# Kernel optimization log

Hardware: AMD Instinct MI355X
Metric: run time of the kernel (lower is better)

The kernel has to match this reference:

```python
import jax, jax.numpy as jnp
import numpy as np

THRESHOLD = 0.75
MIN_TOKENS = 128
POOL_OUT = 128
EPS = 1e-5


def setup_inputs() -> dict:
    key = jax.random.key(0)
    k1, k2 = jax.random.split(key)
    B, T, N, D = 64, 6, 128, 768
    A = 51
    return {
        "features_event": jax.random.normal(k1, (B, T, N, D), dtype=jnp.float32),
        "ln_gamma": jnp.ones((D,), jnp.float32),
        "ln_beta": jnp.zeros((D,), jnp.float32),
        "w_attr": jax.random.normal(k2, (A, D), dtype=jnp.float32) * 0.02,
        "b_attr": jnp.zeros((A,), jnp.float32),
        "bn_gamma": jnp.ones((A,), jnp.float32),
        "bn_beta": jnp.zeros((A,), jnp.float32),
    }


def _filter_and_pool(x):
    # x: [B, TN, D] -> [B, POOL_OUT, D], faithful to
    # filter_similar_tokens_vectorized + pad_sequence + AdaptiveAvgPool1d(128).
    B, TN, D = x.shape
    x_norm = x / jnp.linalg.norm(x, axis=-1, keepdims=True)
    sim = jnp.einsum('bid,bjd->bij', x_norm, x_norm)          # [B, TN, TN]
    high = (sim > THRESHOLD) & ~jnp.eye(TN, dtype=bool)[None]
    keep = ~jnp.any(high, axis=2)                             # [B, TN]
    counts = jnp.sum(keep, axis=1)
    # per-sample fallback: if fewer than MIN_TOKENS survive, keep top-k by L2 norm
    scores = jnp.linalg.norm(x, axis=-1)                      # [B, TN]
    _, topk_idx = jax.lax.top_k(scores, MIN_TOKENS)
    topk_mask = jnp.zeros((B, TN), bool).at[jnp.arange(B)[:, None], topk_idx].set(True)
    keep = jnp.where((counts < MIN_TOKENS)[:, None], topk_mask, keep)
    counts = jnp.sum(keep, axis=1)                            # per-sample kept length
    L = jnp.max(counts)                                       # pad_sequence length (traced scalar)
    # stable compaction: kept tokens first, original order preserved; zeros after
    order = jnp.argsort(~keep, axis=1, stable=True)           # [B, TN]
    xs = jnp.take_along_axis(x, order[:, :, None], axis=1)
    pos = jnp.arange(TN)
    xs = jnp.where(pos[None, :, None] < counts[:, None, None], xs, 0.0)
    # AdaptiveAvgPool1d(POOL_OUT) over the first L columns (zeros beyond each
    # sample's count are included, exactly as torch pools the padded tensor).
    # Identity when L == POOL_OUT (each bin holds exactly one element).
    i = jnp.arange(POOL_OUT)
    start = (i * L) // POOL_OUT
    end = ((i + 1) * L + POOL_OUT - 1) // POOL_OUT            # ceil div
    W = ((pos[None, :] >= start[:, None]) & (pos[None, :] < end[:, None])).astype(x.dtype)
    W = W / (end - start)[:, None].astype(x.dtype)            # [POOL_OUT, TN]
    return jnp.einsum('oj,bjd->bod', W, xs)                   # [B, POOL_OUT, D]


def reference(features_event, ln_gamma, ln_beta, w_attr, b_attr, bn_gamma, bn_beta):
    B, T, N, D = features_event.shape
    x = features_event.reshape(B, T * N, D)
    x = _filter_and_pool(x)                                   # [B, 128, D]
    # LayerNorm(dim)
    mu = jnp.mean(x, axis=-1, keepdims=True)
    var = jnp.var(x, axis=-1, keepdims=True)
    x = (x - mu) * jax.lax.rsqrt(var + EPS) * ln_gamma + ln_beta
    # per-attribute Linear(dim, 1) heads fused into one batched matmul
    A = w_attr.shape[0]
    logits = jnp.einsum('bad,ad->ba', x[:, :A, :], w_attr) + b_attr
    # BatchNorm1d(attr_num), training-mode batch statistics
    bm = jnp.mean(logits, axis=0)
    bv = jnp.var(logits, axis=0)
    return (logits - bm) * jax.lax.rsqrt(bv + EPS) * bn_gamma + bn_beta
```

## Files before the change

kernel.cpp:

```cpp
#include <hip/hip_runtime.h>
#include <hip/hip_bf16.h>

#define TN 768
#define DIM 768
#define NB 64
#define NA 51
#define POOL 128
#define THRESH 0.75f
#define LNEPS 1e-5f

typedef float f32x4 __attribute__((ext_vector_type(4)));
typedef long l64x2 __attribute__((ext_vector_type(2)));

typedef const __attribute__((address_space(1))) unsigned int* gas_p;
typedef __attribute__((address_space(3))) unsigned int* las_p;

__device__ __forceinline__ void gload16(const void* g, void* l) {
    __builtin_amdgcn_global_load_lds((gas_p)g, (las_p)l, 16, 0, 0);
}

__constant__ int PAIR_I[21] = {0,1,1,2,2,2,3,3,3,3,4,4,4,4,4,5,5,5,5,5,5};
__constant__ int PAIR_J[21] = {0,0,1,0,1,2,0,1,2,3,0,1,2,3,4,0,1,2,3,4,5};

__global__ __launch_bounds__(256) void k_norms(const float* __restrict__ x,
                                               unsigned int* __restrict__ xn,
                                               float* __restrict__ norms,
                                               int* __restrict__ bad,
                                               int* __restrict__ Lval) {
    if (blockIdx.x < 192) bad[blockIdx.x * 256 + threadIdx.x] = 0;
    if (blockIdx.x == 0 && threadIdx.x == 0) *Lval = 0;

    const int tok  = blockIdx.x * 4 + (threadIdx.x >> 6);
    const int lane = threadIdx.x & 63;
    const float4* p = (const float4*)(x + (size_t)tok * DIM);
    float4 v[3];
    float s = 0.f;
#pragma unroll
    for (int q = 0; q < 3; ++q) {
        v[q] = p[q * 64 + lane];
        s += v[q].x * v[q].x + v[q].y * v[q].y + v[q].z * v[q].z + v[q].w * v[q].w;
    }
#pragma unroll
    for (int m = 1; m < 64; m <<= 1) s += __shfl_xor(s, m);
    const float nrm = sqrtf(s);
    const float sc = 1.0f / nrm;
    unsigned int* xrow = xn + (size_t)tok * 192;
#pragma unroll
    for (int q = 0; q < 3; ++q) {
        int w0 = __builtin_amdgcn_cvt_pk_fp8_f32(v[q].x * sc, v[q].y * sc, 0, false);
        w0     = __builtin_amdgcn_cvt_pk_fp8_f32(v[q].z * sc, v[q].w * sc, w0, true);
        const int k  = q * 256 + lane * 4;
        const int kb = k & 127;
        const int c  = kb >> 5, sl = (kb >> 3) & 3, r = kb & 7;
        const int pos = (k & ~127) + 16 * (4 * (c >> 1) + sl) + 8 * (c & 1) + r;
        xrow[pos >> 2] = (unsigned)w0;
    }
    if (lane == 0) norms[tok] = nrm;
}

__global__ __launch_bounds__(256) void k_gram(const unsigned char* __restrict__ xn,
                                              int* __restrict__ bad) {
    const int f = blockIdx.x;
    const int lid = (f & 7) * 168 + (f >> 3);
    const int b = lid / 21, p = lid - b * 21;
    const int it = PAIR_I[p], jt = PAIR_J[p];
    const bool diag = (it == jt);

    const int tid = threadIdx.x;
    const int lane = tid & 63, w = tid >> 6;
    const int lr = lane & 15, lt = lane >> 4;
    const int wr = w >> 1, wc = w & 1;

    __shared__ alignas(16) unsigned char lA[2][128 * 128];
    __shared__ alignas(16) unsigned char lB[2][128 * 128];

    const unsigned char* xb = xn + (size_t)b * TN * DIM;
    const int srow = lane >> 3;
    const int sgoff = 16 * ((lane & 7) ^ (srow & 7));
    const size_t baseA = (size_t)(jt * 128 + srow) * DIM + sgoff;
    const size_t baseB = (size_t)(it * 128 + srow) * DIM + sgoff;

    f32x4 acc[4][4];
#pragma unroll
    for (int m = 0; m < 4; ++m)
#pragma unroll
        for (int n = 0; n < 4; ++n) acc[m][n] = {0.f, 0.f, 0.f, 0.f};

    auto stage = [&](int bb, int kk) {
#pragma unroll
        for (int i = 0; i < 4; ++i) {
            const int seg = w * 4 + i;
            gload16(xb + baseA + (size_t)seg * 8 * DIM + kk * 128,
                    (char*)lA[bb] + seg * 1024);
        }
        if (!diag) {
#pragma unroll
            for (int i = 0; i < 4; ++i) {
                const int seg = w * 4 + i;
                gload16(xb + baseB + (size_t)seg * 8 * DIM + kk * 128,
                        (char*)lB[bb] + seg * 1024);
            }
        }
    };

    auto compute = [&](int bb) {
        const unsigned char* As = lA[bb];
        const unsigned char* Bs = diag ? lA[bb] : lB[bb];
        const int gx = lr & 7;
#pragma unroll
        for (int q = 0; q < 2; ++q) {
            const int goff = 16 * ((4 * q + lt) ^ gx);
            l64x2 a[4], bv[4];
#pragma unroll
            for (int m = 0; m < 4; ++m)
                a[m] = *(const l64x2*)&As[(wr * 64 + m * 16 + lr) * 128 + goff];
#pragma unroll
            for (int n = 0; n < 4; ++n)
                bv[n] = *(const l64x2*)&Bs[(wc * 64 + n * 16 + lr) * 128 + goff];
#pragma unroll
            for (int m = 0; m < 4; ++m)
#pragma unroll
                for (int n = 0; n < 4; ++n) {
                    acc[m][n] = __builtin_amdgcn_mfma_f32_16x16x32_fp8_fp8(a[m][0], bv[n][0], acc[m][n], 0, 0, 0);
                    acc[m][n] = __builtin_amdgcn_mfma_f32_16x16x32_fp8_fp8(a[m][1], bv[n][1], acc[m][n], 0, 0, 0);
                }
        }
    };

    stage(0, 0);
    asm volatile("s_waitcnt vmcnt(0)" ::: "memory");
    __builtin_amdgcn_s_barrier();
#pragma unroll
    for (int kk = 0; kk < 6; ++kk) {
        const int cur = kk & 1;
        if (kk < 5) stage(cur ^ 1, kk + 1);
        compute(cur);
        if (kk < 5) {
            asm volatile("s_waitcnt vmcnt(0)" ::: "memory");
            __builtin_amdgcn_s_barrier();
        }
    }

#pragma unroll
    for (int m = 0; m < 4; ++m) {
#pragma unroll
        for (int r = 0; r < 4; ++r) {
            const int rowg = jt * 128 + wr * 64 + m * 16 + lt * 4 + r;
            bool any = false;
#pragma unroll
            for (int n = 0; n < 4; ++n) {
                const int colg = it * 128 + wc * 64 + n * 16 + lr;
                any = any || (acc[m][n][r] > THRESH && rowg != colg);
            }
            if (any) bad[b * TN + rowg] = 1;
        }
    }
    if (!diag) {
#pragma unroll
        for (int n = 0; n < 4; ++n) {
            const int colg = it * 128 + wc * 64 + n * 16 + lr;
            bool any = false;
#pragma unroll
            for (int m = 0; m < 4; ++m)
#pragma unroll
                for (int r = 0; r < 4; ++r)
                    any = any || (acc[m][n][r] > THRESH);
            if (any) bad[b * TN + colg] = 1;
        }
    }
}

__global__ __launch_bounds__(256) void k_filter(const int* __restrict__ bad,
                                                const float* __restrict__ norms,
                                                int* __restrict__ inv,
                                                int* __restrict__ counts,
                                                int* __restrict__ Lval) {
    const int b = blockIdx.x, t = threadIdx.x;
    const int w = t >> 6, l = t & 63;
    __shared__ unsigned long long kw[12];
    __shared__ float nsh[TN];

    bool kp[3];
#pragma unroll
    for (int q = 0; q < 3; ++q)
        kp[q] = (bad[b * TN + q * 256 + w * 64 + l] == 0);
#pragma unroll
    for (int q = 0; q < 3; ++q) {
        unsigned long long m = __ballot(kp[q]);
        if (l == 0) kw[4 * q + w] = m;
    }
    __syncthreads();
    int total = 0;
    for (int i = 0; i < 12; ++i) total += __popcll(kw[i]);

    if (total < POOL) {
        for (int j = t; j < TN; j += 256) nsh[j] = norms[b * TN + j];
        __syncthreads();
#pragma unroll
        for (int q = 0; q < 3; ++q) {
            const int j = q * 256 + w * 64 + l;
            const float nj = nsh[j];
            int rank = 0;
            for (int i = 0; i < TN; ++i) {
                float ni = nsh[i];
                rank += (ni > nj) || (ni == nj && i < j);
            }
            kp[q] = (rank < POOL);
        }
        __syncthreads();
#pragma unroll
        for (int q = 0; q < 3; ++q) {
            unsigned long long m = __ballot(kp[q]);
            if (l == 0) kw[4 * q + w] = m;
        }
        __syncthreads();
        total = 0;
        for (int i = 0; i < 12; ++i) total += __popcll(kw[i]);
    }

#pragma unroll
    for (int q = 0; q < 3; ++q) {
        if (kp[q]) {
            const int W = 4 * q + w;
            int pos = __popcll(kw[W] & ((1ull << l) - 1ull));
            for (int i = 0; i < W; ++i) pos += __popcll(kw[i]);
            inv[b * TN + pos] = q * 256 + w * 64 + l;
        }
    }
    if (t == 0) { counts[b] = total; atomicMax(Lval, total); }
}

__device__ inline float block_sum3(float v, volatile float* sred, int t) {
#pragma unroll
    for (int m = 1; m < 64; m <<= 1) v += __shfl_xor(v, m);
    if ((t & 63) == 0) sred[t >> 6] = v;
    __syncthreads();
    float r = sred[0] + sred[1] + sred[2];
    __syncthreads();
    return r;
}

__global__ __launch_bounds__(192) void k_head(const float* __restrict__ x,
                                              const int* __restrict__ inv,
                                              const int* __restrict__ counts,
                                              const int* __restrict__ Lval,
                                              const float* __restrict__ lng,
                                              const float* __restrict__ lnb,
                                              const float* __restrict__ wat,
                                              const float* __restrict__ bat,
                                              float* __restrict__ logits) {
    const int a = blockIdx.x, b = blockIdx.y, t = threadIdx.x;
    __shared__ float sred[3];
    const int L = *Lval, cnt = counts[b];
    const int start = (a * L) >> 7;
    const int end = ((a + 1) * L + 127) >> 7;
    const int wdt = end - start;
    const int pe = min(end, cnt);
    const int nv = pe - start;

    int idx[7];
#pragma unroll
    for (int i = 0; i < 7; ++i)
        idx[i] = (i < nv) ? inv[b * TN + start + i] : 0;

    float4 v[7];
#pragma unroll
    for (int i = 0; i < 7; ++i)
        if (i < nv)
            v[i] = ((const float4*)(x + (size_t)(b * TN + idx[i]) * DIM))[t];

    float4 s4 = {0.f, 0.f, 0.f, 0.f};
#pragma unroll
    for (int i = 0; i < 7; ++i)
        if (i < nv) {
            s4.x += v[i].x; s4.y += v[i].y; s4.z += v[i].z; s4.w += v[i].w;
        }
    const float iw = 1.0f / (float)wdt;
    s4.x *= iw; s4.y *= iw; s4.z *= iw; s4.w *= iw;

    float s1 = block_sum3(s4.x + s4.y + s4.z + s4.w, sred, t);
    float s2 = block_sum3(s4.x * s4.x + s4.y * s4.y + s4.z * s4.z + s4.w * s4.w, sred, t);
    const float mu = s1 * (1.0f / 768.0f);
    const float var = s2 * (1.0f / 768.0f) - mu * mu;
    const float rstd = rsqrtf(var + LNEPS);

    const float4 g  = ((const float4*)lng)[t];
    const float4 be = ((const float4*)lnb)[t];
    const float4 wv = ((const float4*)(wat + (size_t)a * DIM))[t];
    float d = ((s4.x - mu) * rstd * g.x + be.x) * wv.x
            + ((s4.y - mu) * rstd * g.y + be.y) * wv.y
            + ((s4.z - mu) * rstd * g.z + be.z) * wv.z
            + ((s4.w - mu) * rstd * g.w + be.w) * wv.w;
    float dot = block_sum3(d, sred, t);
    if (t == 0) logits[b * NA + a] = dot + bat[a];
}

__global__ __launch_bounds__(64) void k_bn(const float* __restrict__ logits,
                                           const float* __restrict__ bng,
                                           const float* __restrict__ bnb,
                                           float* __restrict__ out) {
    const int a = threadIdx.x;
    if (a >= NA) return;
    float s = 0.f, s2 = 0.f;
    for (int b = 0; b < NB; ++b) {
        float v = logits[b * NA + a];
        s += v; s2 += v * v;
    }
    const float m = s * (1.0f / 64.0f);
    const float var = s2 * (1.0f / 64.0f) - m * m;
    const float rstd = rsqrtf(var + LNEPS);
    const float ga = bng[a], be = bnb[a];
    for (int b = 0; b < NB; ++b)
        out[b * NA + a] = (logits[b * NA + a] - m) * rstd * ga + be;
}

extern "C" void kernel_launch(void* const* d_in, const int* in_sizes, int n_in,
                              void* d_out, int out_size, void* d_ws, size_t ws_size,
                              hipStream_t stream) {
    const float* x     = (const float*)d_in[0];
    const float* ln_g  = (const float*)d_in[1];
    const float* ln_b  = (const float*)d_in[2];
    const float* w_at  = (const float*)d_in[3];
    const float* b_at  = (const float*)d_in[4];
    const float* bn_g  = (const float*)d_in[5];
    const float* bn_b  = (const float*)d_in[6];
    float* out = (float*)d_out;

    char* wsc = (char*)d_ws;
    const size_t XN = 64ull * 768 * 768;
    unsigned char* xn = (unsigned char*)wsc;
    float* norms  = (float*)(wsc + XN);
    int*   bad    = (int*)(wsc + XN + 196608);
    int*   inv    = (int*)(wsc + XN + 393216);
    int*   counts = (int*)(wsc + XN + 589824);
    int*   Lval   = (int*)(wsc + XN + 590080);
    float* logits = (float*)(wsc + XN + 590336);

    k_norms <<<NB * TN / 4, 256, 0, stream>>>(x, (unsigned int*)xn, norms, bad, Lval);
    k_gram  <<<21 * NB, 256, 0, stream>>>(xn, bad);
    k_filter<<<NB, 256, 0, stream>>>(bad, norms, inv, counts, Lval);
    k_head  <<<dim3(NA, NB), 192, 0, stream>>>(x, inv, counts, Lval,
                                               ln_g, ln_b, w_at, b_at, logits);
    k_bn    <<<1, 64, 0, stream>>>(logits, bn_g, bn_b, out);
}
```

Baseline: 76.98 us.

## Make gram kernel persistent over 2-3 tile pairs with cross-tile prefetch

The Gram kernel now launches 512 blocks instead of one block per tile pair, and each block walks 2 or 3 consecutive (batch, tile-pair) items. While it computes the last K-chunk of one tile it prefetches the first chunk of the next, which hides the per-tile prologue load and evens out the tail across CUs. The fp8 normalized rows are now stored in plain order instead of the permuted MFMA-friendly layout. This is still correct because both operands read the same layout and the dot product ignores a consistent K permutation, and it removes index math in k_norms. The trade-offs are fewer blocks in flight and some serialization of the epilogue inside each block.

```diff
diff --git a/kernel.cpp b/kernel.cpp
--- a/kernel.cpp
+++ b/kernel.cpp
@@ -49,22 +49,19 @@
     for (int q = 0; q < 3; ++q) {
         int w0 = __builtin_amdgcn_cvt_pk_fp8_f32(v[q].x * sc, v[q].y * sc, 0, false);
         w0     = __builtin_amdgcn_cvt_pk_fp8_f32(v[q].z * sc, v[q].w * sc, w0, true);
-        const int k  = q * 256 + lane * 4;
-        const int kb = k & 127;
-        const int c  = kb >> 5, sl = (kb >> 3) & 3, r = kb & 7;
-        const int pos = (k & ~127) + 16 * (4 * (c >> 1) + sl) + 8 * (c & 1) + r;
-        xrow[pos >> 2] = (unsigned)w0;
+        xrow[q * 64 + lane] = (unsigned)w0;
     }
     if (lane == 0) norms[tok] = nrm;
 }
+
+struct PS { const unsigned char* pA; const unsigned char* pB; int b, it, jt, diag; };
 
 __global__ __launch_bounds__(256) void k_gram(const unsigned char* __restrict__ xn,
                                               int* __restrict__ bad) {
-    const int f = blockIdx.x;
-    const int lid = (f & 7) * 168 + (f >> 3);
-    const int b = lid / 21, p = lid - b * 21;
-    const int it = PAIR_I[p], jt = PAIR_J[p];
-    const bool diag = (it == jt);
+    const int blk = blockIdx.x;
+    const int chunk = (blk & 7) * 64 + (blk >> 3);
+    const int np     = (chunk < 320) ? 3 : 2;
+    const int pstart = (chunk < 320) ? chunk * 3 : 960 + (chunk - 320) * 2;
 
     const int tid = threadIdx.x;
     const int lane = tid & 63, w = tid >> 6;
@@ -74,38 +71,40 @@
     __shared__ alignas(16) unsigned char lA[2][128 * 128];
     __shared__ alignas(16) unsigned char lB[2][128 * 128];
 
-    const unsigned char* xb = xn + (size_t)b * TN * DIM;
     const int srow = lane >> 3;
     const int sgoff = 16 * ((lane & 7) ^ (srow & 7));
-    const size_t baseA = (size_t)(jt * 128 + srow) * DIM + sgoff;
-    const size_t baseB = (size_t)(it * 128 + srow) * DIM + sgoff;
-
-    f32x4 acc[4][4];
-#pragma unroll
-    for (int m = 0; m < 4; ++m)
-#pragma unroll
-        for (int n = 0; n < 4; ++n) acc[m][n] = {0.f, 0.f, 0.f, 0.f};
-
-    auto stage = [&](int bb, int kk) {
+
+    auto mkstate = [&](int idx, PS& s) {
+        const int lid = pstart + idx;
+        const int b = lid / 21, p = lid - b * 21;
+        s.b = b; s.it = PAIR_I[p]; s.jt = PAIR_J[p]; s.diag = (s.it == s.jt);
+        const unsigned char* xb = xn + (size_t)b * TN * DIM;
+        s.pA = xb + (size_t)(s.jt * 128 + srow) * DIM + sgoff;
+        s.pB = xb + (size_t)(s.it * 128 + srow) * DIM + sgoff;
+    };
+
+    auto stage = [&](const PS& s, int bb, int kk) {
 #pragma unroll
         for (int i = 0; i < 4; ++i) {
             const int seg = w * 4 + i;
-            gload16(xb + baseA + (size_t)seg * 8 * DIM + kk * 128,
+            gload16(s.pA + (size_t)seg * 8 * DIM + kk * 128,
                     (char*)lA[bb] + seg * 1024);
         }
-        if (!diag) {
+        if (!s.diag) {
 #pragma unroll
             for (int i = 0; i < 4; ++i) {
                 const int seg = w * 4 + i;
-                gload16(xb + baseB + (size_t)seg * 8 * DIM + kk * 128,
+                gload16(s.pB + (size_t)seg * 8 * DIM + kk * 128,
                         (char*)lB[bb] + seg * 1024);
             }
         }
     };
 
-    auto compute = [&](int bb) {
+    f32x4 acc[4][4];
+
+    auto compute = [&](int bb, const PS& s) {
         const unsigned char* As = lA[bb];
-        const unsigned char* Bs = diag ? lA[bb] : lB[bb];
+        const unsigned char* Bs = s.diag ? lA[bb] : lB[bb];
         const int gx = lr & 7;
 #pragma unroll
         for (int q = 0; q < 2; ++q) {
@@ -127,45 +126,67 @@
         }
     };
 
-    stage(0, 0);
+    auto epilogue = [&](const PS& s) {
+#pragma unroll
+        for (int m = 0; m < 4; ++m) {
+#pragma unroll
+            for (int r = 0; r < 4; ++r) {
+                const int rowg = s.jt * 128 + wr * 64 + m * 16 + lt * 4 + r;
+                bool any = false;
+#pragma unroll
+                for (int n = 0; n < 4; ++n) {
+                    const int colg = s.it * 128 + wc * 64 + n * 16 + lr;
+                    any = any || (acc[m][n][r] > THRESH && rowg != colg);
+                }
+                if (any) bad[s.b * TN + rowg] = 1;
+            }
+        }
+        if (!s.diag) {
+#pragma unroll
+            for (int n = 0; n < 4; ++n) {
+                const int colg = s.it * 128 + wc * 64 + n * 16 + lr;
+                bool any = false;
+#pragma unroll
+                for (int m = 0; m < 4; ++m)
+#pragma unroll
+                    for (int r = 0; r < 4; ++r)
+                        any = any || (acc[m][n][r] > THRESH);
+                if (any) bad[s.b * TN + colg] = 1;
+            }
+        }
+    };
+
+    PS cur, nxt;
+    mkstate(0, cur);
+    mkstate(1, nxt);
+    stage(cur, 0, 0);
     asm volatile("s_waitcnt vmcnt(0)" ::: "memory");
     __builtin_amdgcn_s_barrier();
-#pragma unroll
-    for (int kk = 0; kk < 6; ++kk) {
-        const int cur = kk & 1;
-        if (kk < 5) stage(cur ^ 1, kk + 1);
-        compute(cur);
-        if (kk < 5) {
-            asm volatile("s_waitcnt vmcnt(0)" ::: "memory");
-            __builtin_amdgcn_s_barrier();
-        }
-    }
-
-#pragma unroll
-    for (int m = 0; m < 4; ++m) {
-#pragma unroll
-        for (int r = 0; r < 4; ++r) {
-            const int rowg = jt * 128 + wr * 64 + m * 16 + lt * 4 + r;
-            bool any = false;
-#pragma unroll
-            for (int n = 0; n < 4; ++n) {
-                const int colg = it * 128 + wc * 64 + n * 16 + lr;
-                any = any || (acc[m][n][r] > THRESH && rowg != colg);
-            }
-            if (any) bad[b * TN + rowg] = 1;
-        }
-    }
-    if (!diag) {
-#pragma unroll
-        for (int n = 0; n < 4; ++n) {
-            const int colg = it * 128 + wc * 64 + n * 16 + lr;
-            bool any = false;
-#pragma unroll
-            for (int m = 0; m < 4; ++m)
-#pragma unroll
-                for (int r = 0; r < 4; ++r)
-                    any = any || (acc[m][n][r] > THRESH);
-            if (any) bad[b * TN + colg] = 1;
+
+    const int total = np * 6;
+    for (int i = 0; i < np; ++i) {
+#pragma unroll
+        for (int m = 0; m < 4; ++m)
+#pragma unroll
+            for (int n = 0; n < 4; ++n) acc[m][n] = {0.f, 0.f, 0.f, 0.f};
+#pragma unroll
+        for (int kk = 0; kk < 6; ++kk) {
+            const int flat = i * 6 + kk;
+            const bool last = (flat == total - 1);
+            if (!last) {
+                if (kk < 5) stage(cur, (flat + 1) & 1, kk + 1);
+                else        stage(nxt, (flat + 1) & 1, 0);
+            }
+            compute(flat & 1, cur);
+            if (!last) {
+                asm volatile("s_waitcnt vmcnt(0)" ::: "memory");
+                __builtin_amdgcn_s_barrier();
+            }
+        }
+        epilogue(cur);
+        if (i + 1 < np) {
+            cur = nxt;
+            if (i + 2 < np) mkstate(i + 2, nxt);
         }
     }
 }
@@ -337,7 +358,7 @@
     float* logits = (float*)(wsc + XN + 590336);
 
     k_norms <<<NB * TN / 4, 256, 0, stream>>>(x, (unsigned int*)xn, norms, bad, Lval);
-    k_gram  <<<21 * NB, 256, 0, stream>>>(xn, bad);
+    k_gram  <<<512, 256, 0, stream>>>(xn, bad);
     k_filter<<<NB, 256, 0, stream>>>(bad, norms, inv, counts, Lval);
     k_head  <<<dim3(NA, NB), 192, 0, stream>>>(x, inv, counts, Lval,
                                                ln_g, ln_b, w_at, b_at, logits);
```

Measured after the change: 80.06 us. +4.0%, slower.
